# Performance work log

Hardware: AMD Instinct MI355X
Metric: run time of the kernel (lower is better)

## Reference

```python
import jax, jax.numpy as jnp
import numpy as np

LEVELS = 3  # num_basis = 1 + 1 + 2 + 4 = 8


def _haar_basis(x):
    """Closed-form vectorized Haar basis, x: [B, F] raw inputs.

    Replaces the original nested per-feature/per-level/per-bucket mask loops:
    at each level only one bucket k = floor(u*freq) is active, with value
    +2^(level/2) on the left half of the bucket and -2^(level/2) on the right
    half (x == 1.0 falls in the right half of the last bucket, matching the
    torch edge-case handling).
    """
    u = (jnp.tanh(x) + 1.0) / 2.0  # normalize to [0, 1]
    cols = [jnp.ones_like(u)[..., None]]  # scaling function phi
    for level in range(LEVELS):
        freq = 2 ** level
        k = jnp.clip(jnp.floor(u * freq), 0, freq - 1).astype(jnp.int32)  # bucket idx
        mid = (k.astype(u.dtype) + 0.5) / freq
        amp = jnp.asarray(2.0 ** (level / 2), u.dtype)
        sign = jnp.where(u < mid, amp, -amp)  # [B, F]
        cols.append(jax.nn.one_hot(k, freq, dtype=u.dtype) * sign[..., None])
    return jnp.concatenate(cols, axis=-1)  # [B, F, num_basis]


def setup_inputs() -> dict:
    key = jax.random.key(0)
    k1, k2, k3 = jax.random.split(key, 3)
    B, F, O, NB = 32768, 1024, 64, 8
    x = jax.random.normal(k1, (B, F), dtype=jnp.float32)
    coeffs = jax.random.normal(k2, (F, O, NB), dtype=jnp.float32) * 0.05
    base_weight = jax.random.normal(k3, (F, O), dtype=jnp.float32) * 0.05
    return {"x": x, "coeffs": coeffs, "base_weight": base_weight}


def reference(x, coeffs, base_weight):
    basis = _haar_basis(x)                         # [B, F, NB]
    wave_out = jnp.einsum('bin,ion->bo', basis, coeffs)  # [B, O]
    out = wave_out + x @ base_weight               # residual path
    kl = jnp.zeros((1,), dtype=x.dtype)            # non-variational: kl = 0
    return (out, kl)
```

## Files before the change

kernel.cpp:

```cpp
#include <hip/hip_runtime.h>
#include <math.h>


typedef __attribute__((ext_vector_type(8))) short short8;
typedef __attribute__((ext_vector_type(4))) float f32x4;

__device__ __forceinline__ unsigned int f2bf(float f) {
  unsigned int u = __float_as_uint(f);
  u += 0x7FFFu + ((u >> 16) & 1u);
  return u >> 16;
}

__device__ __forceinline__ void gen_basis(int j, unsigned int* d) {
  d[0] = (j < 4) ? 0x3F803F80u : 0xBF803F80u;
  unsigned int sq1 = (j & 2) ? 0xBFB5u : 0x3FB5u;
  d[1] = (j & 4) ? (sq1 << 16) : sq1;
  unsigned long long sd2 = (j & 1) ? 0xC000ull : 0x4000ull;
  unsigned long long d23 = sd2 << ((j & 6) << 3);
  d[2] = (unsigned int)d23;
  d[3] = (unsigned int)(d23 >> 32);
}

#define BARRIER() __asm__ volatile("s_waitcnt lgkmcnt(0)\n\ts_barrier" ::: "memory")

__device__ __forceinline__ void build_chunk(const float4& xa, const float4& xb,
                                            uint4* __restrict__ dst) {
  float xv[8];
  xv[0] = xa.x; xv[1] = xa.y; xv[2] = xa.z; xv[3] = xa.w;
  xv[4] = xb.x; xv[5] = xb.y; xv[6] = xb.z; xv[7] = xb.w;
  float t8v[8];
  unsigned int bad = 0;
#pragma unroll
  for (int ff = 0; ff < 8; ++ff) {
    float e = __expf(2.0f * xv[ff]);
    float r = __builtin_amdgcn_rcpf(e + 1.0f);
    float t8 = __builtin_fmaf(-8.0f, r, 8.0f);
    float rn = rintf(t8);
    if (fabsf(t8 - rn) < 3e-5f) bad |= 1u << ff;
    t8v[ff] = t8;
  }
  if (__builtin_expect(bad != 0, 0)) {
#pragma unroll
    for (int ff = 0; ff < 8; ++ff)
      if (bad & (1u << ff)) {
        float tf = (float)tanh((double)xv[ff]);
        t8v[ff] = ((tf + 1.0f) * 0.5f) * 8.0f;
      }
  }
  unsigned int dw[36];
#pragma unroll
  for (int p = 0; p < 4; ++p) {
    int je = (int)t8v[2 * p];     je = je > 7 ? 7 : je;
    int jo = (int)t8v[2 * p + 1]; jo = jo > 7 ? 7 : jo;
    gen_basis(je, &dw[9 * p]);
    dw[9 * p + 4] = f2bf(xv[2 * p]) | (f2bf(xv[2 * p + 1]) << 16);
    gen_basis(jo, &dw[9 * p + 5]);
  }
#pragma unroll
  for (int gg = 0; gg < 9; ++gg) {
    uint4 qv; qv.x = dw[4 * gg]; qv.y = dw[4 * gg + 1];
    qv.z = dw[4 * gg + 2]; qv.w = dw[4 * gg + 3];
    dst[gg * 256] = qv;
  }
}

__global__ __launch_bounds__(256) void build_w(const float* __restrict__ coeffs,
                                               const float* __restrict__ bw,
                                               uint4* __restrict__ Wsw) {
  const int l = threadIdx.x & 63;
  const int t = threadIdx.x >> 6;
  const int g = blockIdx.x;
  const int c = g / 9, j = g - c * 9;
  const int R = c * 4 + (l >> 4);
  const int o = t * 16 + (l & 15);
  unsigned int dwv[4];
#pragma unroll
  for (int jj = 0; jj < 8; ++jj) {
    int d = 8 * j + jj;
    int p = d / 18;
    int e = d - p * 18;
    int f, n;
    if (e < 8)       { f = 8 * R + 2 * p;     n = e; }
    else if (e == 8) { f = 8 * R + 2 * p;     n = 8; }
    else if (e == 9) { f = 8 * R + 2 * p + 1; n = 8; }
    else             { f = 8 * R + 2 * p + 1; n = e - 10; }
    float v = (n < 8) ? coeffs[(f * 64 + o) * 8 + n] : bw[f * 64 + o];
    unsigned int h = f2bf(v);
    if (jj & 1) dwv[jj >> 1] |= h << 16; else dwv[jj >> 1] = h;
  }
  uint4 qq; qq.x = dwv[0]; qq.y = dwv[1]; qq.z = dwv[2]; qq.w = dwv[3];
  Wsw[(g * 4 + t) * 64 + l] = qq;
}

template <int NS>
__device__ __forceinline__ void run_main(const float* __restrict__ xrow,
                                         const uint4* __restrict__ Wsw,
                                         uint4* __restrict__ Albuf,
                                         f32x4* acc,
                                         int s0, int q, int mm, int bdoff, int l) {
  float4 xa = *(const float4*)(xrow);
  float4 xb = *(const float4*)(xrow + 4);
  build_chunk(xa, xb, Albuf + bdoff);
  xa = *(const float4*)(xrow + 32);
  xb = *(const float4*)(xrow + 36);
  BARRIER();
  for (int c = 0; c < 32; ++c) {
    uint4* cur = Albuf + (c & 1) * 2304;
    uint4* nxt = Albuf + ((c + 1) & 1) * 2304;
    uint4 Bv[NS][4];
#pragma unroll
    for (int i = 0; i < NS; ++i) {
      const uint4* wp = Wsw + (size_t)((c * 9 + s0 + 4 * i) * 256) + l;
      Bv[i][0] = wp[0]; Bv[i][1] = wp[64]; Bv[i][2] = wp[128]; Bv[i][3] = wp[192];
    }
    if (c + 1 < 32) {
      build_chunk(xa, xb, nxt + bdoff);
      if (c + 2 < 32) {
        xa = *(const float4*)(xrow + (c + 2) * 32);
        xb = *(const float4*)(xrow + (c + 2) * 32 + 4);
      }
    }
#pragma unroll
    for (int i = 0; i < NS; ++i) {
      const int sl = s0 + 4 * i;
      const uint4* rb = cur + sl * 256 + q * 64 + mm;
      short8 a0 = __builtin_bit_cast(short8, rb[0]);
      short8 a1 = __builtin_bit_cast(short8, rb[16]);
      short8 a2 = __builtin_bit_cast(short8, rb[32]);
      short8 a3 = __builtin_bit_cast(short8, rb[48]);
#pragma unroll
      for (int t = 0; t < 4; ++t) {
        short8 Bt = __builtin_bit_cast(short8, Bv[i][t]);
        acc[0 * 4 + t] = __builtin_amdgcn_mfma_f32_16x16x32_bf16(a0, Bt, acc[0 * 4 + t], 0, 0, 0);
        acc[1 * 4 + t] = __builtin_amdgcn_mfma_f32_16x16x32_bf16(a1, Bt, acc[1 * 4 + t], 0, 0, 0);
        acc[2 * 4 + t] = __builtin_amdgcn_mfma_f32_16x16x32_bf16(a2, Bt, acc[2 * 4 + t], 0, 0, 0);
        acc[3 * 4 + t] = __builtin_amdgcn_mfma_f32_16x16x32_bf16(a3, Bt, acc[3 * 4 + t], 0, 0, 0);
      }
    }
    BARRIER();
  }
}

__global__ __launch_bounds__(256, 2) void wavelet_gemm(const float* __restrict__ x,
                                                       const uint4* __restrict__ Wsw,
                                                       float* __restrict__ out,
                                                       int out_size) {
  __shared__ uint4 Albuf[2 * 9 * 4 * 64];
  const int tid = threadIdx.x;
  const int l = tid & 63;
  const int w = tid >> 6;
  const int q = l >> 4;
  const int mm = l & 15;
  const int m = tid & 63;
  const int bdoff = w * 64 + m;
  const long rowbase = (long)blockIdx.x * 64;

  f32x4 acc[16];
#pragma unroll
  for (int i = 0; i < 16; ++i) acc[i] = (f32x4){0.f, 0.f, 0.f, 0.f};

  const float* xrow = x + (rowbase + m) * 1024 + w * 8;

  if (w == 0) run_main<3>(xrow, Wsw, Albuf, acc, 0, q, mm, bdoff, l);
  else        run_main<2>(xrow, Wsw, Albuf, acc, w, q, mm, bdoff, l);

  float* P = (float*)Albuf;
  float* W = P + w * 4096;
#pragma unroll
  for (int rt = 0; rt < 4; ++rt)
#pragma unroll
    for (int tt = 0; tt < 4; ++tt)
      *(f32x4*)(W + (16 * tt + mm) * 64 + 16 * rt + 4 * q) = acc[rt * 4 + tt];
  BARRIER();

  const int col = tid & 63;
  float* og = out + (size_t)rowbase * 64;
#pragma unroll
  for (int s = 0; s < 4; ++s) {
    int rg = s * 4 + (tid >> 6);
    f32x4 v = *(f32x4*)(P + 0 * 4096 + col * 64 + 4 * rg);
    v = v + *(f32x4*)(P + 1 * 4096 + col * 64 + 4 * rg);
    v = v + *(f32x4*)(P + 2 * 4096 + col * 64 + 4 * rg);
    v = v + *(f32x4*)(P + 3 * 4096 + col * 64 + 4 * rg);
#pragma unroll
    for (int r = 0; r < 4; ++r)
      og[(4 * rg + r) * 64 + col] = v[r];
  }
  if (blockIdx.x == 0 && tid == 0) out[out_size - 1] = 0.0f;
}

extern "C" void kernel_launch(void* const* d_in, const int* in_sizes, int n_in,
                              void* d_out, int out_size, void* d_ws, size_t ws_size,
                              hipStream_t stream) {
  const float* x      = (const float*)d_in[0];
  const float* coeffs = (const float*)d_in[1];
  const float* bw     = (const float*)d_in[2];
  uint4* Wsw = (uint4*)d_ws;
  float* out = (float*)d_out;

  build_w<<<288, 256, 0, stream>>>(coeffs, bw, Wsw);
  wavelet_gemm<<<512, 256, 0, stream>>>(x, (const uint4*)Wsw, out, out_size);
}
```

Baseline: 232.8 us.

## Replace per-element tanh with host-precomputed bucket thresholds and retile GEMM

```diff
diff --git a/kernel.cpp b/kernel.cpp
--- a/kernel.cpp
+++ b/kernel.cpp
@@ -1,5 +1,6 @@
 #include <hip/hip_runtime.h>
 #include <math.h>
+#include <string.h>
 
 
 typedef __attribute__((ext_vector_type(8))) short short8;
@@ -22,47 +23,6 @@
 }
 
 #define BARRIER() __asm__ volatile("s_waitcnt lgkmcnt(0)\n\ts_barrier" ::: "memory")
-
-__device__ __forceinline__ void build_chunk(const float4& xa, const float4& xb,
-                                            uint4* __restrict__ dst) {
-  float xv[8];
-  xv[0] = xa.x; xv[1] = xa.y; xv[2] = xa.z; xv[3] = xa.w;
-  xv[4] = xb.x; xv[5] = xb.y; xv[6] = xb.z; xv[7] = xb.w;
-  float t8v[8];
-  unsigned int bad = 0;
-#pragma unroll
-  for (int ff = 0; ff < 8; ++ff) {
-    float e = __expf(2.0f * xv[ff]);
-    float r = __builtin_amdgcn_rcpf(e + 1.0f);
-    float t8 = __builtin_fmaf(-8.0f, r, 8.0f);
-    float rn = rintf(t8);
-    if (fabsf(t8 - rn) < 3e-5f) bad |= 1u << ff;
-    t8v[ff] = t8;
-  }
-  if (__builtin_expect(bad != 0, 0)) {
-#pragma unroll
-    for (int ff = 0; ff < 8; ++ff)
-      if (bad & (1u << ff)) {
-        float tf = (float)tanh((double)xv[ff]);
-        t8v[ff] = ((tf + 1.0f) * 0.5f) * 8.0f;
-      }
-  }
-  unsigned int dw[36];
-#pragma unroll
-  for (int p = 0; p < 4; ++p) {
-    int je = (int)t8v[2 * p];     je = je > 7 ? 7 : je;
-    int jo = (int)t8v[2 * p + 1]; jo = jo > 7 ? 7 : jo;
-    gen_basis(je, &dw[9 * p]);
-    dw[9 * p + 4] = f2bf(xv[2 * p]) | (f2bf(xv[2 * p + 1]) << 16);
-    gen_basis(jo, &dw[9 * p + 5]);
-  }
-#pragma unroll
-  for (int gg = 0; gg < 9; ++gg) {
-    uint4 qv; qv.x = dw[4 * gg]; qv.y = dw[4 * gg + 1];
-    qv.z = dw[4 * gg + 2]; qv.w = dw[4 * gg + 3];
-    dst[gg * 256] = qv;
-  }
-}
 
 __global__ __launch_bounds__(256) void build_w(const float* __restrict__ coeffs,
                                                const float* __restrict__ bw,
@@ -92,101 +52,128 @@
   Wsw[(g * 4 + t) * 64 + l] = qq;
 }
 
-template <int NS>
-__device__ __forceinline__ void run_main(const float* __restrict__ xrow,
-                                         const uint4* __restrict__ Wsw,
-                                         uint4* __restrict__ Albuf,
-                                         f32x4* acc,
-                                         int s0, int q, int mm, int bdoff, int l) {
-  float4 xa = *(const float4*)(xrow);
-  float4 xb = *(const float4*)(xrow + 4);
-  build_chunk(xa, xb, Albuf + bdoff);
-  xa = *(const float4*)(xrow + 32);
-  xb = *(const float4*)(xrow + 36);
-  BARRIER();
-  for (int c = 0; c < 32; ++c) {
-    uint4* cur = Albuf + (c & 1) * 2304;
-    uint4* nxt = Albuf + ((c + 1) & 1) * 2304;
-    uint4 Bv[NS][4];
-#pragma unroll
-    for (int i = 0; i < NS; ++i) {
-      const uint4* wp = Wsw + (size_t)((c * 9 + s0 + 4 * i) * 256) + l;
-      Bv[i][0] = wp[0]; Bv[i][1] = wp[64]; Bv[i][2] = wp[128]; Bv[i][3] = wp[192];
-    }
-    if (c + 1 < 32) {
-      build_chunk(xa, xb, nxt + bdoff);
-      if (c + 2 < 32) {
-        xa = *(const float4*)(xrow + (c + 2) * 32);
-        xb = *(const float4*)(xrow + (c + 2) * 32 + 4);
-      }
-    }
-#pragma unroll
-    for (int i = 0; i < NS; ++i) {
-      const int sl = s0 + 4 * i;
-      const uint4* rb = cur + sl * 256 + q * 64 + mm;
-      short8 a0 = __builtin_bit_cast(short8, rb[0]);
-      short8 a1 = __builtin_bit_cast(short8, rb[16]);
-      short8 a2 = __builtin_bit_cast(short8, rb[32]);
-      short8 a3 = __builtin_bit_cast(short8, rb[48]);
-#pragma unroll
-      for (int t = 0; t < 4; ++t) {
-        short8 Bt = __builtin_bit_cast(short8, Bv[i][t]);
-        acc[0 * 4 + t] = __builtin_amdgcn_mfma_f32_16x16x32_bf16(a0, Bt, acc[0 * 4 + t], 0, 0, 0);
-        acc[1 * 4 + t] = __builtin_amdgcn_mfma_f32_16x16x32_bf16(a1, Bt, acc[1 * 4 + t], 0, 0, 0);
-        acc[2 * 4 + t] = __builtin_amdgcn_mfma_f32_16x16x32_bf16(a2, Bt, acc[2 * 4 + t], 0, 0, 0);
-        acc[3 * 4 + t] = __builtin_amdgcn_mfma_f32_16x16x32_bf16(a3, Bt, acc[3 * 4 + t], 0, 0, 0);
-      }
-    }
-    BARRIER();
-  }
-}
-
-__global__ __launch_bounds__(256, 2) void wavelet_gemm(const float* __restrict__ x,
+__global__ __launch_bounds__(256, 4) void wavelet_gemm(const float* __restrict__ x,
                                                        const uint4* __restrict__ Wsw,
                                                        float* __restrict__ out,
-                                                       int out_size) {
-  __shared__ uint4 Albuf[2 * 9 * 4 * 64];
+                                                       int out_size,
+                                                       float4 Ta, float4 Tb) {
+  __shared__ uint4 Albuf[18 * 4 * 32];
   const int tid = threadIdx.x;
   const int l = tid & 63;
   const int w = tid >> 6;
   const int q = l >> 4;
   const int mm = l & 15;
-  const int m = tid & 63;
-  const int bdoff = w * 64 + m;
-  const long rowbase = (long)blockIdx.x * 64;
+  const int m = tid & 31;
+  const int r = tid >> 5;
+  const long rowbase = (long)blockIdx.x * 32;
 
-  f32x4 acc[16];
+  f32x4 acc[8];
 #pragma unroll
-  for (int i = 0; i < 16; ++i) acc[i] = (f32x4){0.f, 0.f, 0.f, 0.f};
+  for (int i = 0; i < 8; ++i) acc[i] = (f32x4){0.f, 0.f, 0.f, 0.f};
 
-  const float* xrow = x + (rowbase + m) * 1024 + w * 8;
+  const float* xrow = x + (rowbase + m) * 1024 + r * 8;
+  const int wboff = ((r >> 2) * 36 + (r & 3)) * 32 + m;
 
-  if (w == 0) run_main<3>(xrow, Wsw, Albuf, acc, 0, q, mm, bdoff, l);
-  else        run_main<2>(xrow, Wsw, Albuf, acc, w, q, mm, bdoff, l);
+  float4 xa = *(const float4*)(xrow);
+  float4 xb = *(const float4*)(xrow + 4);
+
+  for (int sc = 0; sc < 16; ++sc) {
+    float xv[8];
+    xv[0] = xa.x; xv[1] = xa.y; xv[2] = xa.z; xv[3] = xa.w;
+    xv[4] = xb.x; xv[5] = xb.y; xv[6] = xb.z; xv[7] = xb.w;
+    unsigned int dw[36];
+#pragma unroll
+    for (int p = 0; p < 4; ++p) {
+      float xe = xv[2 * p], xo = xv[2 * p + 1];
+      int je = (xe >= Ta.x) + (xe >= Ta.y) + (xe >= Ta.z) + (xe >= Ta.w)
+             + (xe >= Tb.x) + (xe >= Tb.y) + (xe >= Tb.z);
+      int jo = (xo >= Ta.x) + (xo >= Ta.y) + (xo >= Ta.z) + (xo >= Ta.w)
+             + (xo >= Tb.x) + (xo >= Tb.y) + (xo >= Tb.z);
+      gen_basis(je, &dw[9 * p]);
+      dw[9 * p + 4] = f2bf(xe) | (f2bf(xo) << 16);
+      gen_basis(jo, &dw[9 * p + 5]);
+    }
+#pragma unroll
+    for (int gg = 0; gg < 9; ++gg) {
+      uint4 qv; qv.x = dw[4 * gg]; qv.y = dw[4 * gg + 1];
+      qv.z = dw[4 * gg + 2]; qv.w = dw[4 * gg + 3];
+      Albuf[wboff + gg * 128] = qv;
+    }
+    BARRIER();
+    if (sc + 1 < 16) {
+      xa = *(const float4*)(xrow + (sc + 1) * 64);
+      xb = *(const float4*)(xrow + (sc + 1) * 64 + 4);
+    }
+    const int t = w ^ ((sc & 1) << 1);
+    const int NS = (t < 2) ? 5 : 4;
+    for (int i = 0; i < NS; ++i) {
+      const int s = t + 4 * i;
+      const uint4* ab = Albuf + (s * 4 + q) * 32 + mm;
+      short8 a0 = __builtin_bit_cast(short8, ab[0]);
+      short8 a1 = __builtin_bit_cast(short8, ab[16]);
+      const uint4* wp = Wsw + (size_t)(sc * 18 + s) * 256 + l;
+      short8 b0 = __builtin_bit_cast(short8, wp[0]);
+      short8 b1 = __builtin_bit_cast(short8, wp[64]);
+      short8 b2 = __builtin_bit_cast(short8, wp[128]);
+      short8 b3 = __builtin_bit_cast(short8, wp[192]);
+      acc[0] = __builtin_amdgcn_mfma_f32_16x16x32_bf16(a0, b0, acc[0], 0, 0, 0);
+      acc[1] = __builtin_amdgcn_mfma_f32_16x16x32_bf16(a0, b1, acc[1], 0, 0, 0);
+      acc[2] = __builtin_amdgcn_mfma_f32_16x16x32_bf16(a0, b2, acc[2], 0, 0, 0);
+      acc[3] = __builtin_amdgcn_mfma_f32_16x16x32_bf16(a0, b3, acc[3], 0, 0, 0);
+      acc[4] = __builtin_amdgcn_mfma_f32_16x16x32_bf16(a1, b0, acc[4], 0, 0, 0);
+      acc[5] = __builtin_amdgcn_mfma_f32_16x16x32_bf16(a1, b1, acc[5], 0, 0, 0);
+      acc[6] = __builtin_amdgcn_mfma_f32_16x16x32_bf16(a1, b2, acc[6], 0, 0, 0);
+      acc[7] = __builtin_amdgcn_mfma_f32_16x16x32_bf16(a1, b3, acc[7], 0, 0, 0);
+    }
+    BARRIER();
+  }
 
   float* P = (float*)Albuf;
-  float* W = P + w * 4096;
 #pragma unroll
-  for (int rt = 0; rt < 4; ++rt)
-#pragma unroll
-    for (int tt = 0; tt < 4; ++tt)
-      *(f32x4*)(W + (16 * tt + mm) * 64 + 16 * rt + 4 * q) = acc[rt * 4 + tt];
+  for (int s = 0; s < 8; ++s)
+    *(f32x4*)(P + w * 2048 + s * 256 + 4 * l) = acc[s];
   BARRIER();
-
-  const int col = tid & 63;
   float* og = out + (size_t)rowbase * 64;
 #pragma unroll
-  for (int s = 0; s < 4; ++s) {
-    int rg = s * 4 + (tid >> 6);
-    f32x4 v = *(f32x4*)(P + 0 * 4096 + col * 64 + 4 * rg);
-    v = v + *(f32x4*)(P + 1 * 4096 + col * 64 + 4 * rg);
-    v = v + *(f32x4*)(P + 2 * 4096 + col * 64 + 4 * rg);
-    v = v + *(f32x4*)(P + 3 * 4096 + col * 64 + 4 * rg);
+  for (int si = 0; si < 2; ++si) {
+    const int s = 2 * w + si;
+    f32x4 v = *(f32x4*)(P + 0 * 2048 + s * 256 + 4 * l);
+    v = v + *(f32x4*)(P + 1 * 2048 + s * 256 + 4 * l);
+    v = v + *(f32x4*)(P + 2 * 2048 + s * 256 + 4 * l);
+    v = v + *(f32x4*)(P + 3 * 2048 + s * 256 + 4 * l);
+    const int rt = s >> 2, tt = s & 3;
 #pragma unroll
-    for (int r = 0; r < 4; ++r)
-      og[(4 * rg + r) * 64 + col] = v[r];
+    for (int e = 0; e < 4; ++e)
+      og[(16 * rt + 4 * q + e) * 64 + 16 * tt + mm] = v[e];
   }
   if (blockIdx.x == 0 && tid == 0) out[out_size - 1] = 0.0f;
+}
+
+static unsigned int f32key(float f) {
+  unsigned int u; memcpy(&u, &f, 4);
+  return (u & 0x80000000u) ? ~u : (u | 0x80000000u);
+}
+static float f32unkey(unsigned int k) {
+  unsigned int u = (k & 0x80000000u) ? (k ^ 0x80000000u) : ~k;
+  float f; memcpy(&f, &u, 4);
+  return f;
+}
+static bool pipe_ge(float x, int k) {
+  float tf = (float)tanh((double)x);
+  float s = (tf + 1.0f) * 0.5f;
+  float t8 = s * 8.0f;
+  return t8 >= (float)k;
+}
+static void thresholds(float* X) {
+  for (int k = 1; k <= 7; ++k) {
+    unsigned int lo = f32key(-4.0f);
+    unsigned int hi = f32key(4.0f);
+    while (hi - lo > 1) {
+      unsigned int mid = lo + (hi - lo) / 2;
+      if (pipe_ge(f32unkey(mid), k)) hi = mid; else lo = mid;
+    }
+    X[k - 1] = f32unkey(hi);
+  }
 }
 
 extern "C" void kernel_launch(void* const* d_in, const int* in_sizes, int n_in,
@@ -198,6 +185,11 @@
   uint4* Wsw = (uint4*)d_ws;
   float* out = (float*)d_out;
 
+  float X[7];
+  thresholds(X);
+  float4 Ta; Ta.x = X[0]; Ta.y = X[1]; Ta.z = X[2]; Ta.w = X[3];
+  float4 Tb; Tb.x = X[4]; Tb.y = X[5]; Tb.z = X[6]; Tb.w = 1e30f;
+
   build_w<<<288, 256, 0, stream>>>(coeffs, bw, Wsw);
-  wavelet_gemm<<<512, 256, 0, stream>>>(x, (const uint4*)Wsw, out, out_size);
+  wavelet_gemm<<<1024, 256, 0, stream>>>(x, (const uint4*)Wsw, out, out_size, Ta, Tb);
 }
```

New measurement: 248.8 us. 6.9% more time.
